# Kernel optimization log

Measured on AMD Instinct MI355X. Metric: run time of the kernel, lower is better.

## Reference

```python
import jax, jax.numpy as jnp
import numpy as np

ROTARY_BASE = 10000
INFTY_APPROX = 1e30
B, T, M, H, D = 2, 2048, 2048, 16, 128


def rope(x):
    # x: [B, T, H, D]; half-split rotary encoding
    *_, length, _, width = x.shape
    half = width // 2
    positions = jnp.arange(length, dtype=jnp.float32)[None, :, None, None]      # [1,T,1,1]
    dims = jnp.arange(half, dtype=jnp.float32)
    ang_freqs = jnp.power(float(ROTARY_BASE), -dims / half)[None, None, None, :]  # [1,1,1,D/2]
    radians = positions * ang_freqs
    cos = jnp.cos(radians).astype(x.dtype)
    sin = jnp.sin(radians).astype(x.dtype)
    even, odd = x[..., :half], x[..., half:]
    r_even = even * cos - odd * sin
    r_odd = even * sin + odd * cos
    return jnp.concatenate([r_even, r_odd], axis=-1)


def setup_inputs() -> dict:
    key = jax.random.key(0)
    k0, k1, k2, k3, k4 = jax.random.split(key, 5)
    return {
        "x": jax.random.normal(k0, (B, T, M), dtype=jnp.float32),
        "w_aq": jax.random.normal(k1, (H, M, D), dtype=jnp.float32) * (M ** -0.5),
        "w_ak": jax.random.normal(k2, (H, M, D), dtype=jnp.float32) * (M ** -0.5),
        "w_av": jax.random.normal(k3, (H, M, D), dtype=jnp.float32) * (M ** -0.5),
        "w_ao": jax.random.normal(k4, (H, D, M), dtype=jnp.float32) * ((2 * 24 * M) ** -0.5),
    }


def reference(x, w_aq, w_ak, w_av, w_ao):
    q = jnp.einsum("btm,hmd->bthd", x, w_aq)
    k = jnp.einsum("btm,hmd->bthd", x, w_ak)
    v = jnp.einsum("btm,hmd->bthd", x, w_av)
    q = rope(q)
    k = rope(k)
    # muP attention scaling: 1/d_head (not 1/sqrt(d_head))
    mult = (1.0 / D) ** 0.5
    s = jnp.einsum("bihd,bjhd->bhij", mult * q, mult * k)  # [B,H,T,T]
    i = jnp.arange(T)[:, None]
    j = jnp.arange(T)[None, :]
    mask = (i < j)[None, None, :, :]  # mask future positions
    s = s - jnp.asarray(INFTY_APPROX, dtype=x.dtype) * mask
    p = jax.nn.softmax(s, axis=-1)
    o = jnp.einsum("bhij,bjhd->bihd", p, v)
    r = jnp.einsum("bihd,hdm->bim", o, w_ao)
    return r
```

## Files before the change

kernel.cpp:

```cpp
#include <hip/hip_runtime.h>

#define Bb 2
#define Tt 2048
#define Mm 2048
#define Hh 16
#define Dd 128

typedef __attribute__((ext_vector_type(8))) short bf16x8;
typedef __attribute__((ext_vector_type(4))) float f32x4;
typedef __attribute__((ext_vector_type(16))) float f32x16;

__device__ __forceinline__ unsigned short f2bf(float f) {
    unsigned int u = __builtin_bit_cast(unsigned int, f);
    u += 0x7FFFu + ((u >> 16) & 1u);
    return (unsigned short)(u >> 16);
}

__device__ __forceinline__ unsigned int cvt_pk_bf16(float lo, float hi) {
    unsigned int r;
    asm("v_cvt_pk_bf16_f32 %0, %1, %2" : "=v"(r) : "v"(lo), "v"(hi));
    return r;
}

__device__ __forceinline__ float fexp2(float x) { return __builtin_amdgcn_exp2f(x); }

__device__ __forceinline__ void gld16(const void* g, void* l) {
    __builtin_amdgcn_global_load_lds(
        (const __attribute__((address_space(1))) void*)g,
        (__attribute__((address_space(3))) void*)l, 16, 0, 0);
}


__global__ __launch_bounds__(256) void cvt_x_kernel(const float* __restrict__ x,
                                                    unsigned short* __restrict__ xb) {
    long i = ((long)blockIdx.x * 256 + threadIdx.x) * 4;
    float4 v = *(const float4*)(x + i);
    unsigned short r0 = f2bf(v.x), r1 = f2bf(v.y), r2 = f2bf(v.z), r3 = f2bf(v.w);
    unsigned int lo = (unsigned int)r0 | ((unsigned int)r1 << 16);
    unsigned int hi = (unsigned int)r2 | ((unsigned int)r3 << 16);
    uint2 packed; packed.x = lo; packed.y = hi;
    *(uint2*)(xb + i) = packed;
}

__global__ __launch_bounds__(256) void transpose_cvt(const float* __restrict__ in,
                                                     unsigned short* __restrict__ out,
                                                     int rows, int cols,
                                                     long in_slab, long out_slab) {
    __shared__ float tile[32][33];
    const float* ip = in + (long)blockIdx.z * in_slab;
    unsigned short* op = out + (long)blockIdx.z * out_slab;
    int r0 = blockIdx.x * 32, c0 = blockIdx.y * 32;
    int tx = threadIdx.x & 31, ty = threadIdx.x >> 5;
#pragma unroll
    for (int j = 0; j < 32; j += 8)
        tile[ty + j][tx] = ip[(long)(r0 + ty + j) * cols + c0 + tx];
    __syncthreads();
#pragma unroll
    for (int j = 0; j < 32; j += 8)
        op[(long)(c0 + ty + j) * rows + r0 + tx] = f2bf(tile[tx][ty + j]);
}

__global__ __launch_bounds__(256) void transpose_cvt_qkv(
    const float* __restrict__ wq, const float* __restrict__ wk, const float* __restrict__ wv,
    unsigned short* __restrict__ outBase) {
    __shared__ float tile[32][33];
    const int z = blockIdx.z;
    const int which = z >> 4, slab = z & 15;
    const float* ip = (which == 0 ? wq : which == 1 ? wk : wv) + (long)slab * 2048 * 128;
    unsigned short* op = outBase + (long)which * 4194304 + (long)slab * 128 * 2048;
    int r0 = blockIdx.x * 32, c0 = blockIdx.y * 32;
    int tx = threadIdx.x & 31, ty = threadIdx.x >> 5;
#pragma unroll
    for (int j = 0; j < 32; j += 8)
        tile[ty + j][tx] = ip[(long)(r0 + ty + j) * 128 + c0 + tx];
    __syncthreads();
#pragma unroll
    for (int j = 0; j < 32; j += 8) {
        int d = c0 + ty + j;
        int ord = (d >> 6) + 2 * ((d >> 5) & 1);
        int p = (d & 31) + 32 * ord;
        op[(long)p * 2048 + r0 + tx] = f2bf(tile[tx][ty + j]);
    }
}

__global__ __launch_bounds__(256) void rope_tab(float* __restrict__ cosT,
                                                float* __restrict__ sinT) {
    int idx = blockIdx.x * 256 + threadIdx.x;
    int t = idx >> 6, d = idx & 63;
    float freq = powf(10000.f, -(float)d / 64.f);
    float ang = (float)t * freq;
    sinT[idx] = sinf(ang);
    cosT[idx] = cosf(ang);
}

__global__ __launch_bounds__(256, 2) void proj_gemm3(
    const unsigned short* __restrict__ xb,
    const unsigned short* __restrict__ wqT,
    const unsigned short* __restrict__ wkT,
    const unsigned short* __restrict__ wvT,
    unsigned short* __restrict__ qO,
    unsigned short* __restrict__ kO,
    unsigned short* __restrict__ vtO,
    const float* __restrict__ cosT,
    const float* __restrict__ sinT) {
    __shared__ __align__(16) char lds[49152];
    const int bm = blockIdx.x;
    const int bn = blockIdx.y;
    const int off = bn * 256;
    const int mode = off >> 11;
    const unsigned short* wT = (mode == 0) ? wqT : (mode == 1) ? wkT : wvT;
    const unsigned short* Asrc = xb + (long)bm * 128 * Mm;
    const unsigned short* Bsrc = wT + (long)(off & 2047) * Mm;

    const int tid = threadIdx.x, lane = tid & 63, wave = tid >> 6;
    const int il = lane & 31, hl = lane >> 5;
    const int wm = wave >> 1, wn = wave & 1;

    f32x16 acc[2][4];
#pragma unroll
    for (int a = 0; a < 2; ++a)
#pragma unroll
        for (int b2 = 0; b2 < 4; ++b2)
#pragma unroll
            for (int e = 0; e < 16; ++e) acc[a][b2][e] = 0.f;

    for (int kt = 0; kt < 32; ++kt) {
#pragma unroll
        for (int l = 0; l < 4; ++l) {
            int f = l * 256 + tid;
            int r = f >> 3, c = f & 7;
            gld16(Asrc + (long)r * Mm + kt * 64 + ((c ^ (r & 7)) << 3), lds + f * 16);
        }
#pragma unroll
        for (int l = 0; l < 8; ++l) {
            int f = l * 256 + tid;
            int s = f >> 8, q = f & 255, rr = q >> 3, c = q & 7;
            gld16(Bsrc + (long)(s * 32 + rr) * Mm + kt * 64 + ((c ^ (rr & 7)) << 3),
                  lds + 16384 + f * 16);
        }
        asm volatile("s_waitcnt vmcnt(0)" ::: "memory");
        __builtin_amdgcn_s_barrier();

#pragma unroll
        for (int kk = 0; kk < 4; ++kk) {
            bf16x8 af[2], bf[4];
#pragma unroll
            for (int mf = 0; mf < 2; ++mf) {
                int row = wm * 64 + mf * 32 + il;
                af[mf] = *(const bf16x8*)(lds + row * 128 + (((kk * 2 + hl) ^ (row & 7)) << 4));
            }
#pragma unroll
            for (int nf = 0; nf < 4; ++nf) {
                int st = wn * 4 + nf;
                bf[nf] = *(const bf16x8*)(lds + 16384 + st * 4096 + il * 128 +
                                          (((kk * 2 + hl) ^ (il & 7)) << 4));
            }
            __builtin_amdgcn_s_setprio(1);
#pragma unroll
            for (int mf = 0; mf < 2; ++mf)
#pragma unroll
                for (int nf = 0; nf < 4; ++nf)
                    acc[mf][nf] = __builtin_amdgcn_mfma_f32_32x32x16_bf16(af[mf], bf[nf], acc[mf][nf], 0, 0, 0);
            __builtin_amdgcn_s_setprio(0);
        }
        asm volatile("" ::: "memory");
        __builtin_amdgcn_s_barrier();
    }

    const int b = bm >> 4;
    const int t0 = (bm & 15) * 128;
    const int head = ((off & 2047) >> 7) + wn;

    if (mode < 2) {
        const float qs = (mode == 0) ? 0.011271055f : 1.0f;
        unsigned short* outp = (mode == 0) ? qO : kO;
        long hb = ((long)(b * Hh + head)) * Tt;
#pragma unroll
        for (int mf = 0; mf < 2; ++mf)
#pragma unroll
            for (int np = 0; np < 2; ++np) {
                int d_lo = il + 32 * np;
#pragma unroll
                for (int reg = 0; reg < 16; ++reg) {
                    int r = (reg & 3) + 8 * (reg >> 2) + 4 * hl;
                    int t = t0 + wm * 64 + mf * 32 + r;
                    float c = cosT[t * 64 + d_lo], s = sinT[t * 64 + d_lo];
                    float ev = acc[mf][np * 2][reg], od = acc[mf][np * 2 + 1][reg];
                    long base = (hb + t) * Dd;
                    outp[base + d_lo]      = f2bf((ev * c - od * s) * qs);
                    outp[base + d_lo + 64] = f2bf((ev * s + od * c) * qs);
                }
            }
    } else {
        char* patch = lds + wave * 8192;
        long hdbase = ((long)(b * Hh + head)) * Dd;
#pragma unroll
        for (int mf = 0; mf < 2; ++mf) {
#pragma unroll
            for (int nf = 0; nf < 4; ++nf) {
                int dslot = nf * 32 + il;
                int swz = (dslot & 3) << 4;
#pragma unroll
                for (int qg = 0; qg < 4; ++qg) {
                    uint2 w;
                    w.x = cvt_pk_bf16(acc[mf][nf][qg * 4 + 0], acc[mf][nf][qg * 4 + 1]);
                    w.y = cvt_pk_bf16(acc[mf][nf][qg * 4 + 2], acc[mf][nf][qg * 4 + 3]);
                    *(uint2*)(patch + dslot * 64 + ((qg * 16 + hl * 8) ^ swz)) = w;
                }
            }
            __builtin_amdgcn_s_waitcnt(0);
#pragma unroll
            for (int p = 0; p < 8; ++p) {
                int dslot = p * 16 + (lane >> 2);
                int t8 = lane & 3;
                uint4 v = *(const uint4*)(patch + dslot * 64 + ((t8 * 16) ^ ((dslot & 3) << 4)));
                int ordv = dslot >> 5, il2 = dslot & 31;
                int d = il2 + 32 * (ordv >> 1) + 64 * (ordv & 1);
                int tg = t0 + wm * 64 + mf * 32 + t8 * 8;
                *(uint4*)(vtO + (hdbase + d) * Tt + tg) = v;
            }
            __builtin_amdgcn_s_waitcnt(0);
        }
    }
}

__global__ __launch_bounds__(256) void attn_kernel(
    const unsigned short* __restrict__ q,
    const unsigned short* __restrict__ k,
    const unsigned short* __restrict__ vt,
    unsigned short* __restrict__ o) {
    __shared__ __align__(16) unsigned short lds[32768];

    const int lid = (int)blockIdx.x;
    const int p = lid & 255;
    const int bh = p & 31;
    const int q0 = p >> 5;
    const int qb = (lid >> 8) ? (15 - q0) : q0;

    const int tid = threadIdx.x, lane = tid & 63, wave = tid >> 6;
    const int h = lane >> 5, iln = lane & 31;

    const unsigned short* qp = q + (long)bh * Tt * Dd;
    const unsigned short* kp = k + (long)bh * Tt * Dd;
    const unsigned short* vp = vt + (long)bh * Dd * Tt;

    const int i_g = qb * 128 + wave * 32 + iln;
    bf16x8 qf[8];
#pragma unroll
    for (int kk = 0; kk < 8; ++kk)
        qf[kk] = *(const bf16x8*)(qp + (long)i_g * Dd + kk * 16 + h * 8);

    f32x16 accO[4];
#pragma unroll
    for (int nb = 0; nb < 4; ++nb)
#pragma unroll
        for (int e = 0; e < 16; ++e) accO[nb][e] = 0.f;

    float m_r = -1e30f, l_r = 0.f;
    const int ntiles = 2 * qb + 2;

    auto stage = [&](int buf, int tix) {
        const int j0s = tix * 64;
#pragma unroll
        for (int it = 0; it < 4; ++it) {
            int f = it * 256 + tid;
            int rk = f >> 4, ck = f & 15;
            gld16(kp + ((long)(j0s + rk) * Dd + ((ck ^ (rk & 7)) << 3)),
                  (char*)lds + buf * 16384 + f * 16);
            int rv = f >> 3, cv = f & 7;
            gld16(vp + ((long)rv * Tt + j0s + ((cv ^ (rv & 7)) << 3)),
                  (char*)lds + 32768 + buf * 16384 + f * 16);
        }
    };

    stage(0, 0);

    for (int tix = 0; tix < ntiles; ++tix) {
        const int cur = tix & 1;
        const int j0 = tix * 64;
        if (tix + 1 < ntiles) {
            stage(cur ^ 1, tix + 1);
            asm volatile("s_waitcnt vmcnt(8)" ::: "memory");
        } else {
            asm volatile("s_waitcnt vmcnt(0)" ::: "memory");
        }
        __builtin_amdgcn_s_barrier();

        const char* Kb = (const char*)lds + cur * 16384;
        const char* Vb = (const char*)lds + 32768 + cur * 16384;

        f32x16 sacc[2];
#pragma unroll
        for (int mb = 0; mb < 2; ++mb)
#pragma unroll
            for (int e = 0; e < 16; ++e) sacc[mb][e] = 0.f;

        __builtin_amdgcn_s_setprio(1);
#pragma unroll
        for (int mb = 0; mb < 2; ++mb) {
            int row = mb * 32 + iln;
            const char* Kr = Kb + row * 256;
            int sw = row & 7;
#pragma unroll
            for (int kk = 0; kk < 8; ++kk) {
                bf16x8 kf = *(const bf16x8*)(Kr + 16 * ((kk * 2 + h) ^ sw));
                sacc[mb] = __builtin_amdgcn_mfma_f32_32x32x16_bf16(kf, qf[kk], sacc[mb], 0, 0, 0);
            }
        }
        __builtin_amdgcn_s_setprio(0);

        const bool domask = (j0 + 63 > qb * 128);
        if (domask) {
#pragma unroll
            for (int mb = 0; mb < 2; ++mb)
#pragma unroll
                for (int reg = 0; reg < 16; ++reg) {
                    int j = j0 + mb * 32 + (reg & 3) + 8 * (reg >> 2) + 4 * h;
                    if (j > i_g) sacc[mb][reg] = -1e30f;
                }
        }

        float red[16];
#pragma unroll
        for (int r = 0; r < 16; ++r) red[r] = fmaxf(sacc[0][r], sacc[1][r]);
#pragma unroll
        for (int s = 8; s >= 1; s >>= 1)
#pragma unroll
            for (int r = 0; r < s; ++r) red[r] = fmaxf(red[r], red[r + s]);
        float mx = fmaxf(red[0], __shfl_xor(red[0], 32, 64));

        if (__any(mx > m_r + 8.f)) {
            float mn = fmaxf(m_r, mx);
            float corr = fexp2(m_r - mn);
            m_r = mn;
            l_r *= corr;
#pragma unroll
            for (int reg = 0; reg < 16; ++reg) {
                int rrow = (reg & 3) + 8 * (reg >> 2) + 4 * h;
                float c = __shfl(corr, rrow, 64);
#pragma unroll
                for (int nb = 0; nb < 4; ++nb) accO[nb][reg] *= c;
            }
        }

        float pe[2][16];
#pragma unroll
        for (int mb = 0; mb < 2; ++mb)
#pragma unroll
            for (int r = 0; r < 16; ++r) pe[mb][r] = fexp2(sacc[mb][r] - m_r);
        float sr[16];
#pragma unroll
        for (int r = 0; r < 16; ++r) sr[r] = pe[0][r] + pe[1][r];
#pragma unroll
        for (int s = 8; s >= 1; s >>= 1)
#pragma unroll
            for (int r = 0; r < s; ++r) sr[r] += sr[r + s];
        l_r += sr[0] + __shfl_xor(sr[0], 32, 64);

        unsigned int pu[2][8];
#pragma unroll
        for (int mb = 0; mb < 2; ++mb)
#pragma unroll
            for (int t = 0; t < 8; ++t)
                pu[mb][t] = cvt_pk_bf16(pe[mb][2 * t], pe[mb][2 * t + 1]);

        unsigned int rv2[2][4];
#pragma unroll
        for (int mb = 0; mb < 2; ++mb)
#pragma unroll
            for (int u = 0; u < 4; ++u) {
                unsigned int sv = h ? pu[mb][(u & 1) + 4 * (u >> 1)]
                                    : pu[mb][2 + (u & 1) + 4 * (u >> 1)];
                rv2[mb][u] = __shfl_xor(sv, 32, 64);
            }

        __builtin_amdgcn_s_setprio(1);
#pragma unroll
        for (int kk2 = 0; kk2 < 4; ++kk2) {
            const int mb = kk2 >> 1, c2 = kk2 & 1;
            unsigned int w0 = h ? rv2[mb][2 * c2 + 0] : pu[mb][4 * c2 + 0];
            unsigned int w1 = h ? rv2[mb][2 * c2 + 1] : pu[mb][4 * c2 + 1];
            unsigned int w2 = h ? pu[mb][4 * c2 + 2] : rv2[mb][2 * c2 + 0];
            unsigned int w3 = h ? pu[mb][4 * c2 + 3] : rv2[mb][2 * c2 + 1];
            uint4 aw; aw.x = w0; aw.y = w1; aw.z = w2; aw.w = w3;
            bf16x8 af = __builtin_bit_cast(bf16x8, aw);
#pragma unroll
            for (int nb = 0; nb < 4; ++nb) {
                int d = nb * 32 + iln;
                int byte = d * 128 + 16 * ((kk2 * 2 + h) ^ (d & 7));
                bf16x8 vf = *(const bf16x8*)(Vb + byte);
                accO[nb] = __builtin_amdgcn_mfma_f32_32x32x16_bf16(af, vf, accO[nb], 0, 0, 0);
            }
        }
        __builtin_amdgcn_s_setprio(0);

        asm volatile("" ::: "memory");
        __builtin_amdgcn_s_barrier();
    }

    const int b = bh >> 4, hh = bh & 15;
    float invl = 1.f / l_r;
#pragma unroll
    for (int reg = 0; reg < 16; ++reg) {
        int rrow = (reg & 3) + 8 * (reg >> 2) + 4 * h;
        float iv = __shfl(invl, rrow, 64);
        int t = qb * 128 + wave * 32 + rrow;
        long base = ((long)(b * Tt + t) * Hh + hh) * Dd;
#pragma unroll
        for (int nb = 0; nb < 4; ++nb)
            o[base + nb * 32 + iln] = f2bf(accO[nb][reg] * iv);
    }
}

__global__ __launch_bounds__(256, 2) void out_gemm3(
    const unsigned short* __restrict__ oIn,
    const unsigned short* __restrict__ woT,
    float* __restrict__ out) {
    __shared__ __align__(16) char lds[32768];
    const int bm = blockIdx.x, bn = blockIdx.y;
    const int tid = threadIdx.x, lane = tid & 63, wave = tid >> 6;
    const int il = lane & 31, hl = lane >> 5;
    const int wm = wave >> 1, wn = wave & 1;

    const unsigned short* Asrc = oIn + (long)bm * 128 * Mm;
    const unsigned short* Bsrc = woT + (long)bn * 128 * Mm;

    f32x16 acc[2][2];
#pragma unroll
    for (int a = 0; a < 2; ++a)
#pragma unroll
        for (int b2 = 0; b2 < 2; ++b2)
#pragma unroll
            for (int e = 0; e < 16; ++e) acc[a][b2][e] = 0.f;

    for (int kt = 0; kt < 32; ++kt) {
#pragma unroll
        for (int l = 0; l < 4; ++l) {
            int f = l * 256 + tid;
            int r = f >> 3, c = f & 7;
            long koff = kt * 64 + ((c ^ (r & 7)) << 3);
            gld16(Asrc + (long)r * Mm + koff, lds + f * 16);
            gld16(Bsrc + (long)r * Mm + koff, lds + 16384 + f * 16);
        }
        asm volatile("s_waitcnt vmcnt(0)" ::: "memory");
        __builtin_amdgcn_s_barrier();

#pragma unroll
        for (int kk = 0; kk < 4; ++kk) {
            bf16x8 af[2], bf[2];
#pragma unroll
            for (int mf = 0; mf < 2; ++mf) {
                int row = wm * 64 + mf * 32 + il;
                af[mf] = *(const bf16x8*)(lds + row * 128 + (((kk * 2 + hl) ^ (row & 7)) << 4));
            }
#pragma unroll
            for (int nf = 0; nf < 2; ++nf) {
                int col = wn * 64 + nf * 32 + il;
                bf[nf] = *(const bf16x8*)(lds + 16384 + col * 128 +
                                          (((kk * 2 + hl) ^ (col & 7)) << 4));
            }
            __builtin_amdgcn_s_setprio(1);
#pragma unroll
            for (int mf = 0; mf < 2; ++mf)
#pragma unroll
                for (int nf = 0; nf < 2; ++nf)
                    acc[mf][nf] = __builtin_amdgcn_mfma_f32_32x32x16_bf16(af[mf], bf[nf], acc[mf][nf], 0, 0, 0);
            __builtin_amdgcn_s_setprio(0);
        }
        asm volatile("" ::: "memory");
        __builtin_amdgcn_s_barrier();
    }

#pragma unroll
    for (int mf = 0; mf < 2; ++mf)
#pragma unroll
        for (int nf = 0; nf < 2; ++nf)
#pragma unroll
            for (int reg = 0; reg < 16; ++reg) {
                int r = (reg & 3) + 8 * (reg >> 2) + 4 * hl;
                long row = bm * 128 + wm * 64 + mf * 32 + r;
                int col = bn * 128 + wn * 64 + nf * 32 + il;
                out[row * Mm + col] = acc[mf][nf][reg];
            }
}


extern "C" void kernel_launch(void* const* d_in, const int* in_sizes, int n_in,
                              void* d_out, int out_size, void* d_ws, size_t ws_size,
                              hipStream_t stream) {
    const float* x    = (const float*)d_in[0];
    const float* w_aq = (const float*)d_in[1];
    const float* w_ak = (const float*)d_in[2];
    const float* w_av = (const float*)d_in[3];
    const float* w_ao = (const float*)d_in[4];
    float* out = (float*)d_out;

    char* ws = (char*)d_ws;
    const long SZ_BTM = 16777216;
    const long SZ_W   = 8388608;
    unsigned short* xb  = (unsigned short*)(ws);
    unsigned short* qB  = (unsigned short*)(ws + SZ_BTM);
    unsigned short* kB  = (unsigned short*)(ws + 2 * SZ_BTM);
    unsigned short* vtB = (unsigned short*)(ws + 3 * SZ_BTM);
    unsigned short* oB  = (unsigned short*)(ws + 4 * SZ_BTM);
    unsigned short* wqT = (unsigned short*)(ws + 5 * SZ_BTM);
    unsigned short* wkT = (unsigned short*)(ws + 5 * SZ_BTM + SZ_W);
    unsigned short* wvT = (unsigned short*)(ws + 5 * SZ_BTM + 2 * SZ_W);
    unsigned short* woT = (unsigned short*)(ws + 5 * SZ_BTM + 3 * SZ_W);
    float* cosT = (float*)(ws + 5 * SZ_BTM + 4 * SZ_W);
    float* sinT = (float*)(ws + 5 * SZ_BTM + 4 * SZ_W + 524288);

    cvt_x_kernel<<<8192, 256, 0, stream>>>(x, xb);
    transpose_cvt_qkv<<<dim3(64, 4, 48), 256, 0, stream>>>(w_aq, w_ak, w_av, wqT);
    transpose_cvt<<<dim3(64, 64, 1), 256, 0, stream>>>(w_ao, woT, 2048, 2048, 0, 0);
    rope_tab<<<512, 256, 0, stream>>>(cosT, sinT);

    proj_gemm3<<<dim3(32, 24), 256, 0, stream>>>(xb, wqT, wkT, wvT, qB, kB, vtB, cosT, sinT);
    attn_kernel<<<dim3(512), 256, 0, stream>>>(qB, kB, vtB, oB);
    out_gemm3<<<dim3(32, 16), 256, 0, stream>>>(oB, woT, out);
}
```

Before: 276.3 us.

## Pre-tile x and QKV weights into MFMA fragment order; double-buffer output GEMM

The conversion kernels now write x and the QKV weights in bf16 already arranged in per-tile MFMA fragment order. The projection GEMM can then load LDS contiguously and read fragments linearly, with no swizzle arithmetic. The output projection GEMM is rewritten to double-buffer its LDS tiles, prefetching the next K tile while computing the current one. It also switches to 16x16x32 MFMA with a wave-row tiling. This trades some extra prep-kernel complexity and LDS usage (64KB for out_gemm, which limits occupancy) for less address math and better load/compute overlap.

```diff
diff --git a/kernel.cpp b/kernel.cpp
--- a/kernel.cpp
+++ b/kernel.cpp
@@ -31,15 +31,65 @@
 }
 
 
-__global__ __launch_bounds__(256) void cvt_x_kernel(const float* __restrict__ x,
-                                                    unsigned short* __restrict__ xb) {
-    long i = ((long)blockIdx.x * 256 + threadIdx.x) * 4;
-    float4 v = *(const float4*)(x + i);
-    unsigned short r0 = f2bf(v.x), r1 = f2bf(v.y), r2 = f2bf(v.z), r3 = f2bf(v.w);
-    unsigned int lo = (unsigned int)r0 | ((unsigned int)r1 << 16);
-    unsigned int hi = (unsigned int)r2 | ((unsigned int)r3 << 16);
-    uint2 packed; packed.x = lo; packed.y = hi;
-    *(uint2*)(xb + i) = packed;
+__global__ __launch_bounds__(256) void cvt_x2(const float* __restrict__ x,
+                                              unsigned short* __restrict__ xb2) {
+    const int blk = blockIdx.x;
+    const int mt = blk >> 5, kt = blk & 31;
+#pragma unroll
+    for (int it = 0; it < 4; ++it) {
+        int s = it * 256 + threadIdx.x;
+        int row = ((s >> 6) & 3) * 32 + (s & 31);
+        int k = (s >> 8) * 16 + ((s >> 5) & 1) * 8;
+        const float* sp = x + ((long)(mt * 128 + row)) * 2048 + kt * 64 + k;
+        float4 a = *(const float4*)sp;
+        float4 b = *(const float4*)(sp + 4);
+        uint4 pk;
+        pk.x = (unsigned int)f2bf(a.x) | ((unsigned int)f2bf(a.y) << 16);
+        pk.y = (unsigned int)f2bf(a.z) | ((unsigned int)f2bf(a.w) << 16);
+        pk.z = (unsigned int)f2bf(b.x) | ((unsigned int)f2bf(b.y) << 16);
+        pk.w = (unsigned int)f2bf(b.z) | ((unsigned int)f2bf(b.w) << 16);
+        *(uint4*)(xb2 + (((long)(mt * 32 + kt)) * 1024 + s) * 8) = pk;
+    }
+}
+
+__global__ __launch_bounds__(256) void w_qkv_tile(
+    const float* __restrict__ wq, const float* __restrict__ wk, const float* __restrict__ wv,
+    unsigned short* __restrict__ outBase) {
+    __shared__ float tile[64][132];
+    const int kt = blockIdx.x;
+    const int zy = blockIdx.y;
+    const int which = zy >> 4, head = zy & 15;
+    const float* src = (which == 0 ? wq : which == 1 ? wk : wv) + (long)head * 2048 * 128;
+    const int tid = threadIdx.x;
+#pragma unroll
+    for (int it = 0; it < 8; ++it) {
+        int f = it * 256 + tid;
+        int row = f >> 5, c4 = f & 31;
+        float4 v = *(const float4*)(src + (long)(kt * 64 + row) * 128 + c4 * 4);
+        tile[row][c4 * 4 + 0] = v.x;
+        tile[row][c4 * 4 + 1] = v.y;
+        tile[row][c4 * 4 + 2] = v.z;
+        tile[row][c4 * 4 + 3] = v.w;
+    }
+    __syncthreads();
+    const int ntile = head >> 1, wn = head & 1;
+    unsigned short* outp = outBase + (long)which * 4194304 +
+                           ((long)(ntile * 32 + kt)) * 2048 * 8;
+#pragma unroll
+    for (int it = 0; it < 4; ++it) {
+        int up = it * 256 + tid;
+        int kk = up >> 8, nf = (up >> 6) & 3, l = up & 63;
+        int il = l & 31, hl = l >> 5;
+        int d = il + 64 * (nf & 1) + 32 * (nf >> 1);
+        int kl = kk * 16 + hl * 8;
+        uint4 pk;
+        pk.x = (unsigned int)f2bf(tile[kl + 0][d]) | ((unsigned int)f2bf(tile[kl + 1][d]) << 16);
+        pk.y = (unsigned int)f2bf(tile[kl + 2][d]) | ((unsigned int)f2bf(tile[kl + 3][d]) << 16);
+        pk.z = (unsigned int)f2bf(tile[kl + 4][d]) | ((unsigned int)f2bf(tile[kl + 5][d]) << 16);
+        pk.w = (unsigned int)f2bf(tile[kl + 6][d]) | ((unsigned int)f2bf(tile[kl + 7][d]) << 16);
+        int u = kk * 512 + (wn * 4 + nf) * 64 + l;
+        *(uint4*)(outp + (long)u * 8) = pk;
+    }
 }
 
 __global__ __launch_bounds__(256) void transpose_cvt(const float* __restrict__ in,
@@ -60,29 +110,6 @@
         op[(long)(c0 + ty + j) * rows + r0 + tx] = f2bf(tile[tx][ty + j]);
 }
 
-__global__ __launch_bounds__(256) void transpose_cvt_qkv(
-    const float* __restrict__ wq, const float* __restrict__ wk, const float* __restrict__ wv,
-    unsigned short* __restrict__ outBase) {
-    __shared__ float tile[32][33];
-    const int z = blockIdx.z;
-    const int which = z >> 4, slab = z & 15;
-    const float* ip = (which == 0 ? wq : which == 1 ? wk : wv) + (long)slab * 2048 * 128;
-    unsigned short* op = outBase + (long)which * 4194304 + (long)slab * 128 * 2048;
-    int r0 = blockIdx.x * 32, c0 = blockIdx.y * 32;
-    int tx = threadIdx.x & 31, ty = threadIdx.x >> 5;
-#pragma unroll
-    for (int j = 0; j < 32; j += 8)
-        tile[ty + j][tx] = ip[(long)(r0 + ty + j) * 128 + c0 + tx];
-    __syncthreads();
-#pragma unroll
-    for (int j = 0; j < 32; j += 8) {
-        int d = c0 + ty + j;
-        int ord = (d >> 6) + 2 * ((d >> 5) & 1);
-        int p = (d & 31) + 32 * ord;
-        op[(long)p * 2048 + r0 + tx] = f2bf(tile[tx][ty + j]);
-    }
-}
-
 __global__ __launch_bounds__(256) void rope_tab(float* __restrict__ cosT,
                                                 float* __restrict__ sinT) {
     int idx = blockIdx.x * 256 + threadIdx.x;
@@ -93,11 +120,9 @@
     cosT[idx] = cosf(ang);
 }
 
-__global__ __launch_bounds__(256, 2) void proj_gemm3(
-    const unsigned short* __restrict__ xb,
-    const unsigned short* __restrict__ wqT,
-    const unsigned short* __restrict__ wkT,
-    const unsigned short* __restrict__ wvT,
+__global__ __launch_bounds__(256, 2) void proj_gemm4(
+    const unsigned short* __restrict__ xb2,
+    const unsigned short* __restrict__ wT2,
     unsigned short* __restrict__ qO,
     unsigned short* __restrict__ kO,
     unsigned short* __restrict__ vtO,
@@ -106,11 +131,9 @@
     __shared__ __align__(16) char lds[49152];
     const int bm = blockIdx.x;
     const int bn = blockIdx.y;
-    const int off = bn * 256;
-    const int mode = off >> 11;
-    const unsigned short* wT = (mode == 0) ? wqT : (mode == 1) ? wkT : wvT;
-    const unsigned short* Asrc = xb + (long)bm * 128 * Mm;
-    const unsigned short* Bsrc = wT + (long)(off & 2047) * Mm;
+    const int mode = bn >> 3, ntile = bn & 7;
+    const unsigned short* Asrc = xb2 + ((long)bm * 32) * 1024 * 8;
+    const unsigned short* Bsrc = wT2 + (long)mode * 4194304 + ((long)ntile * 32) * 2048 * 8;
 
     const int tid = threadIdx.x, lane = tid & 63, wave = tid >> 6;
     const int il = lane & 31, hl = lane >> 5;
@@ -127,16 +150,13 @@
     for (int kt = 0; kt < 32; ++kt) {
 #pragma unroll
         for (int l = 0; l < 4; ++l) {
-            int f = l * 256 + tid;
-            int r = f >> 3, c = f & 7;
-            gld16(Asrc + (long)r * Mm + kt * 64 + ((c ^ (r & 7)) << 3), lds + f * 16);
+            int s = l * 256 + tid;
+            gld16(Asrc + ((long)kt * 1024 + s) * 8, lds + s * 16);
         }
 #pragma unroll
         for (int l = 0; l < 8; ++l) {
-            int f = l * 256 + tid;
-            int s = f >> 8, q = f & 255, rr = q >> 3, c = q & 7;
-            gld16(Bsrc + (long)(s * 32 + rr) * Mm + kt * 64 + ((c ^ (rr & 7)) << 3),
-                  lds + 16384 + f * 16);
+            int u = l * 256 + tid;
+            gld16(Bsrc + ((long)kt * 2048 + u) * 8, lds + 16384 + u * 16);
         }
         asm volatile("s_waitcnt vmcnt(0)" ::: "memory");
         __builtin_amdgcn_s_barrier();
@@ -145,16 +165,11 @@
         for (int kk = 0; kk < 4; ++kk) {
             bf16x8 af[2], bf[4];
 #pragma unroll
-            for (int mf = 0; mf < 2; ++mf) {
-                int row = wm * 64 + mf * 32 + il;
-                af[mf] = *(const bf16x8*)(lds + row * 128 + (((kk * 2 + hl) ^ (row & 7)) << 4));
-            }
-#pragma unroll
-            for (int nf = 0; nf < 4; ++nf) {
-                int st = wn * 4 + nf;
-                bf[nf] = *(const bf16x8*)(lds + 16384 + st * 4096 + il * 128 +
-                                          (((kk * 2 + hl) ^ (il & 7)) << 4));
-            }
+            for (int mf = 0; mf < 2; ++mf)
+                af[mf] = *(const bf16x8*)(lds + (kk * 256 + (wm * 2 + mf) * 64 + lane) * 16);
+#pragma unroll
+            for (int nf = 0; nf < 4; ++nf)
+                bf[nf] = *(const bf16x8*)(lds + 16384 + (kk * 512 + (wn * 4 + nf) * 64 + lane) * 16);
             __builtin_amdgcn_s_setprio(1);
 #pragma unroll
             for (int mf = 0; mf < 2; ++mf)
@@ -169,7 +184,7 @@
 
     const int b = bm >> 4;
     const int t0 = (bm & 15) * 128;
-    const int head = ((off & 2047) >> 7) + wn;
+    const int head = ntile * 2 + wn;
 
     if (mode < 2) {
         const float qs = (mode == 0) ? 0.011271055f : 1.0f;
@@ -412,76 +427,87 @@
     }
 }
 
-__global__ __launch_bounds__(256, 2) void out_gemm3(
+__global__ __launch_bounds__(256) void out_gemm(
     const unsigned short* __restrict__ oIn,
     const unsigned short* __restrict__ woT,
     float* __restrict__ out) {
-    __shared__ __align__(16) char lds[32768];
+    __shared__ __align__(16) unsigned short smem[32768];
     const int bm = blockIdx.x, bn = blockIdx.y;
-    const int tid = threadIdx.x, lane = tid & 63, wave = tid >> 6;
-    const int il = lane & 31, hl = lane >> 5;
-    const int wm = wave >> 1, wn = wave & 1;
-
-    const unsigned short* Asrc = oIn + (long)bm * 128 * Mm;
-    const unsigned short* Bsrc = woT + (long)bn * 128 * Mm;
-
-    f32x16 acc[2][2];
+    const int tid = threadIdx.x;
+    const int lane = tid & 63;
+    const int wave = tid >> 6;
+    const int g = lane >> 4;
+    const int ln = lane & 15;
+
+    const unsigned short* arow = oIn + (long)bm * 128 * Mm;
+    const unsigned short* brow = woT + (long)bn * 128 * Mm;
+
+    f32x4 acc[2][8];
 #pragma unroll
     for (int a = 0; a < 2; ++a)
 #pragma unroll
-        for (int b2 = 0; b2 < 2; ++b2)
-#pragma unroll
-            for (int e = 0; e < 16; ++e) acc[a][b2][e] = 0.f;
-
-    for (int kt = 0; kt < 32; ++kt) {
-#pragma unroll
-        for (int l = 0; l < 4; ++l) {
-            int f = l * 256 + tid;
+        for (int b2 = 0; b2 < 8; ++b2)
+#pragma unroll
+            for (int e = 0; e < 4; ++e) acc[a][b2][e] = 0.f;
+
+    auto stage = [&](int buf, int kt) {
+        const int k0 = kt * 64;
+#pragma unroll
+        for (int it = 0; it < 4; ++it) {
+            int f = it * 256 + tid;
             int r = f >> 3, c = f & 7;
-            long koff = kt * 64 + ((c ^ (r & 7)) << 3);
-            gld16(Asrc + (long)r * Mm + koff, lds + f * 16);
-            gld16(Bsrc + (long)r * Mm + koff, lds + 16384 + f * 16);
-        }
-        asm volatile("s_waitcnt vmcnt(0)" ::: "memory");
+            long off = (long)r * Mm + k0 + ((c ^ (r & 7)) << 3);
+            gld16(arow + off, (char*)smem + buf * 32768 + f * 16);
+            gld16(brow + off, (char*)smem + buf * 32768 + 16384 + f * 16);
+        }
+    };
+
+    stage(0, 0);
+
+    for (int kt = 0; kt < Mm / 64; ++kt) {
+        const int cur = kt & 1;
+        if (kt + 1 < Mm / 64) {
+            stage(cur ^ 1, kt + 1);
+            asm volatile("s_waitcnt vmcnt(8)" ::: "memory");
+        } else {
+            asm volatile("s_waitcnt vmcnt(0)" ::: "memory");
+        }
         __builtin_amdgcn_s_barrier();
 
-#pragma unroll
-        for (int kk = 0; kk < 4; ++kk) {
-            bf16x8 af[2], bf[2];
-#pragma unroll
-            for (int mf = 0; mf < 2; ++mf) {
-                int row = wm * 64 + mf * 32 + il;
-                af[mf] = *(const bf16x8*)(lds + row * 128 + (((kk * 2 + hl) ^ (row & 7)) << 4));
-            }
-#pragma unroll
-            for (int nf = 0; nf < 2; ++nf) {
-                int col = wn * 64 + nf * 32 + il;
-                bf[nf] = *(const bf16x8*)(lds + 16384 + col * 128 +
-                                          (((kk * 2 + hl) ^ (col & 7)) << 4));
-            }
-            __builtin_amdgcn_s_setprio(1);
-#pragma unroll
-            for (int mf = 0; mf < 2; ++mf)
-#pragma unroll
-                for (int nf = 0; nf < 2; ++nf)
-                    acc[mf][nf] = __builtin_amdgcn_mfma_f32_32x32x16_bf16(af[mf], bf[nf], acc[mf][nf], 0, 0, 0);
-            __builtin_amdgcn_s_setprio(0);
+        const char* Ab = (const char*)smem + cur * 32768;
+        const char* Bv = Ab + 16384;
+#pragma unroll
+        for (int kc = 0; kc < 2; ++kc) {
+            bf16x8 af[2];
+#pragma unroll
+            for (int rf = 0; rf < 2; ++rf) {
+                int row = wave * 32 + rf * 16 + ln;
+                int byte = (row * 128 + kc * 64 + g * 16) ^ ((row & 7) << 4);
+                af[rf] = *(const bf16x8*)(Ab + byte);
+            }
+#pragma unroll
+            for (int ni = 0; ni < 8; ++ni) {
+                int row = ni * 16 + ln;
+                int byte = (row * 128 + kc * 64 + g * 16) ^ ((row & 7) << 4);
+                bf16x8 bfv = *(const bf16x8*)(Bv + byte);
+#pragma unroll
+                for (int rf = 0; rf < 2; ++rf)
+                    acc[rf][ni] = __builtin_amdgcn_mfma_f32_16x16x32_bf16(af[rf], bfv, acc[rf][ni], 0, 0, 0);
+            }
         }
         asm volatile("" ::: "memory");
         __builtin_amdgcn_s_barrier();
     }
 
 #pragma unroll
-    for (int mf = 0; mf < 2; ++mf)
-#pragma unroll
-        for (int nf = 0; nf < 2; ++nf)
-#pragma unroll
-            for (int reg = 0; reg < 16; ++reg) {
-                int r = (reg & 3) + 8 * (reg >> 2) + 4 * hl;
-                long row = bm * 128 + wm * 64 + mf * 32 + r;
-                int col = bn * 128 + wn * 64 + nf * 32 + il;
-                out[row * Mm + col] = acc[mf][nf][reg];
-            }
+    for (int rf = 0; rf < 2; ++rf)
+#pragma unroll
+        for (int reg = 0; reg < 4; ++reg) {
+            long row = bm * 128 + wave * 32 + rf * 16 + g * 4 + reg;
+#pragma unroll
+            for (int ni = 0; ni < 8; ++ni)
+                out[row * Mm + bn * 128 + ni * 16 + ln] = acc[rf][ni][reg];
+        }
 }
 
 
@@ -498,24 +524,22 @@
     char* ws = (char*)d_ws;
     const long SZ_BTM = 16777216;
     const long SZ_W   = 8388608;
-    unsigned short* xb  = (unsigned short*)(ws);
+    unsigned short* xb2 = (unsigned short*)(ws);
     unsigned short* qB  = (unsigned short*)(ws + SZ_BTM);
     unsigned short* kB  = (unsigned short*)(ws + 2 * SZ_BTM);
     unsigned short* vtB = (unsigned short*)(ws + 3 * SZ_BTM);
     unsigned short* oB  = (unsigned short*)(ws + 4 * SZ_BTM);
-    unsigned short* wqT = (unsigned short*)(ws + 5 * SZ_BTM);
-    unsigned short* wkT = (unsigned short*)(ws + 5 * SZ_BTM + SZ_W);
-    unsigned short* wvT = (unsigned short*)(ws + 5 * SZ_BTM + 2 * SZ_W);
+    unsigned short* wT2 = (unsigned short*)(ws + 5 * SZ_BTM);
     unsigned short* woT = (unsigned short*)(ws + 5 * SZ_BTM + 3 * SZ_W);
     float* cosT = (float*)(ws + 5 * SZ_BTM + 4 * SZ_W);
     float* sinT = (float*)(ws + 5 * SZ_BTM + 4 * SZ_W + 524288);
 
-    cvt_x_kernel<<<8192, 256, 0, stream>>>(x, xb);
-    transpose_cvt_qkv<<<dim3(64, 4, 48), 256, 0, stream>>>(w_aq, w_ak, w_av, wqT);
+    cvt_x2<<<1024, 256, 0, stream>>>(x, xb2);
+    w_qkv_tile<<<dim3(32, 48), 256, 0, stream>>>(w_aq, w_ak, w_av, wT2);
     transpose_cvt<<<dim3(64, 64, 1), 256, 0, stream>>>(w_ao, woT, 2048, 2048, 0, 0);
     rope_tab<<<512, 256, 0, stream>>>(cosT, sinT);
 
-    proj_gemm3<<<dim3(32, 24), 256, 0, stream>>>(xb, wqT, wkT, wvT, qB, kB, vtB, cosT, sinT);
+    proj_gemm4<<<dim3(32, 24), 256, 0, stream>>>(xb2, wT2, qB, kB, vtB, cosT, sinT);
     attn_kernel<<<dim3(512), 256, 0, stream>>>(qB, kB, vtB, oB);
-    out_gemm3<<<dim3(32, 16), 256, 0, stream>>>(oB, woT, out);
-}
+    out_gemm<<<dim3(32, 16), 256, 0, stream>>>(oB, woT, out);
+}
```

After: 267.9 us. 1.03x faster.
